# Optimization experiments

Measured on AMD Instinct MI355X. Metric: run time of the kernel, lower is better.

The kernel has to match this reference:

```python
import jax, jax.numpy as jnp
import numpy as np

S = 2048      # words in the sentence
LMAX = 16     # max chars per word (padded)
VOCAB = 50000
ALPHA = 256
CE = 256      # char_embedding_dim (also char-LSTM hidden)
WE = 512      # word_embedding_dim
H = 1024      # hidden_dim of word LSTM


def setup_inputs() -> dict:
    key = jax.random.key(0)
    ks = jax.random.split(key, 13)
    def u(k, shape, scale):
        return jax.random.uniform(k, shape, jnp.float32, -scale, scale)
    sc_c = 1.0 / np.sqrt(CE).astype(np.float32)   # torch LSTM init scale
    sc_w = 1.0 / np.sqrt(H).astype(np.float32)
    return {
        "word_idxs": jax.random.randint(ks[0], (S,), 0, VOCAB),
        "char_idxs": jax.random.randint(ks[1], (S, LMAX), 0, ALPHA),
        "char_lens": jax.random.randint(ks[2], (S,), 1, LMAX + 1),
        "char_emb": jax.random.normal(ks[3], (ALPHA, CE), jnp.float32) * 0.1,
        "word_emb": jax.random.normal(ks[4], (VOCAB, WE), jnp.float32) * 0.1,
        "Wih_c": u(ks[5], (4 * CE, CE), sc_c),
        "Whh_c": u(ks[6], (4 * CE, CE), sc_c),
        "bih_c": u(ks[7], (4 * CE,), sc_c),
        "bhh_c": u(ks[8], (4 * CE,), sc_c),
        "Wih_w": u(ks[9], (4 * H, WE + CE), sc_w),
        "Whh_w": u(ks[10], (4 * H, H), sc_w),
        "bih_w": u(ks[11], (4 * H,), sc_w),
        "bhh_w": u(ks[12], (4 * H,), sc_w),
    }


def _lstm_scan(xs, Wih, Whh, bih, bhh, hdim):
    """Single-layer LSTM, torch gate order (i, f, g, o). xs: [T, B, D] -> hs [T, B, hdim]."""
    B = xs.shape[1]
    bias = bih + bhh
    def step(carry, x):
        h, c = carry
        gates = x @ Wih.T + h @ Whh.T + bias  # [B, 4*hdim]
        i, f, g, o = jnp.split(gates, 4, axis=-1)
        c = jax.nn.sigmoid(f) * c + jax.nn.sigmoid(i) * jnp.tanh(g)
        h = jax.nn.sigmoid(o) * jnp.tanh(c)
        return (h, c), h
    init = (jnp.zeros((B, hdim), xs.dtype), jnp.zeros((B, hdim), xs.dtype))
    _, hs = jax.lax.scan(step, init, xs)
    return hs


def reference(word_idxs, char_idxs, char_lens, char_emb, word_emb,
              Wih_c, Whh_c, bih_c, bhh_c, Wih_w, Whh_w, bih_w, bhh_w):
    # Char LSTM: batch all S words together (fuses the per-word Python loop).
    # Causality makes output at t = len-1 identical to running the true-length seq.
    ce = char_emb[char_idxs]                  # [S, LMAX, CE]
    ce = jnp.swapaxes(ce, 0, 1)               # [LMAX, S, CE] time-major
    hs = _lstm_scan(ce, Wih_c, Whh_c, bih_c, bhh_c, CE)   # [LMAX, S, CE]
    hs = jnp.swapaxes(hs, 0, 1)               # [S, LMAX, CE]
    last = jnp.take_along_axis(hs, (char_lens - 1)[:, None, None], axis=1)[:, 0]  # [S, CE]

    we = word_emb[word_idxs]                  # [S, WE]
    lstm_in = jnp.concatenate([we, last], axis=-1)[:, None, :]  # [S, 1, WE+CE]
    out = _lstm_scan(lstm_in, Wih_w, Whh_w, bih_w, bhh_w, H)    # [S, 1, H]
    # dropout p=0.0 -> identity
    return out
```

## Files before the change

kernel.cpp:

```cpp
#include <hip/hip_runtime.h>
#include <stdint.h>

#define S_WORDS 2048
#define LMAX    16
#define CE      256
#define WE      512
#define HDIM    1024
#define GC      1024
#define GW      4096
#define KW      768
#define NWG_RNN 128
#define NWB_WIN 512
#define NMIR    4
#define RING_U64 (3 * HDIM)

#define IN_GATES_OFF 0
#define LAST_OFF     33554432
#define WT2C_OFF     35651584
#define WT2W_OFF     37748736
#define RING_OFF     WT2C_OFF
#define FLAGS_OFF    (RING_OFF + NMIR * RING_U64 * 8)

typedef float f32x4 __attribute__((ext_vector_type(4)));

#define LD_AGENT(p) __hip_atomic_load((p), __ATOMIC_RELAXED, __HIP_MEMORY_SCOPE_AGENT)

static __device__ __forceinline__ float sigm(float x) { return 1.0f / (1.0f + __expf(-x)); }
static __device__ __forceinline__ float tanh_fast(float x) {
    float ax = fminf(fabsf(x), 15.0f);
    float e  = __expf(2.0f * ax);
    float t  = (e - 1.0f) / (e + 1.0f);
    return copysignf(t, x);
}

__global__ void prep_c_kernel(const float* __restrict__ Wih,
                              const float* __restrict__ Whh,
                              float2* __restrict__ WT2c) {
    int idx = blockIdx.x * blockDim.x + threadIdx.x;
    if (idx >= 256 * GC) return;
    int kp = idx >> 10, row = idx & (GC - 1);
    int k = kp * 2;
    float2 v;
    if (k < CE) { v.x = Wih[row * CE + k];      v.y = Wih[row * CE + k + 1]; }
    else        { v.x = Whh[row * CE + k - CE]; v.y = Whh[row * CE + k - CE + 1]; }
    WT2c[idx] = v;
}

__global__ void prep_w_kernel(const float* __restrict__ Wih,
                              float2* __restrict__ WT2w) {
    int idx = blockIdx.x * blockDim.x + threadIdx.x;
    if (idx >= 384 * GW) return;
    int kp = idx >> 12, row = idx & (GW - 1);
    float2 v;
    v.x = Wih[row * KW + 2 * kp];
    v.y = Wih[row * KW + 2 * kp + 1];
    WT2w[idx] = v;
}

__global__ void __launch_bounds__(1024, 1) char_lstm_kernel(
    const int* __restrict__ char_idxs,
    const int* __restrict__ char_lens,
    const float* __restrict__ char_emb,
    const float* __restrict__ bih,
    const float* __restrict__ bhh,
    const float2* __restrict__ WT2c,
    float* __restrict__ last_out)
{
    __shared__ float xh[8][2 * CE];
    __shared__ float gex[4][256][9];
    const int j = threadIdx.x & 255;
    const int g = threadIdx.x >> 8;
    const int wbase = blockIdx.x * 8;

    const float bias = bih[g * CE + j] + bhh[g * CE + j];

    int len[2];
    float c[2] = {0.0f, 0.0f};
    len[0] = char_lens[wbase + 2 * g];
    len[1] = char_lens[wbase + 2 * g + 1];
    xh[2 * g][CE + j]     = 0.0f;
    xh[2 * g + 1][CE + j] = 0.0f;

    const float2* __restrict__ wrow = WT2c + g * CE + j;

    for (int t = 0; t < LMAX; t++) {
        {
            int ci0 = char_idxs[(wbase + 2 * g) * LMAX + t];
            int ci1 = char_idxs[(wbase + 2 * g + 1) * LMAX + t];
            xh[2 * g][j]     = char_emb[ci0 * CE + j];
            xh[2 * g + 1][j] = char_emb[ci1 * CE + j];
        }
        __syncthreads();

        float acc[8];
        #pragma unroll
        for (int w = 0; w < 8; w++) acc[w] = 0.0f;

        #pragma unroll 2
        for (int kq = 0; kq < 128; kq++) {
            float2 wv0 = wrow[(size_t)(2 * kq) * GC];
            float2 wv1 = wrow[(size_t)(2 * kq + 1) * GC];
            #pragma unroll
            for (int w = 0; w < 8; w++) {
                f32x4 xv = *(const f32x4*)&xh[w][4 * kq];
                acc[w] = fmaf(wv0.x, xv[0],
                         fmaf(wv0.y, xv[1],
                         fmaf(wv1.x, xv[2],
                         fmaf(wv1.y, xv[3], acc[w]))));
            }
        }

        #pragma unroll
        for (int w = 0; w < 8; w++) gex[g][j][w] = acc[w] + bias;
        __syncthreads();

        #pragma unroll
        for (int ww = 0; ww < 2; ww++) {
            int w = 2 * g + ww;
            float gi = gex[0][j][w];
            float gf = gex[1][j][w];
            float gg = gex[2][j][w];
            float go = gex[3][j][w];
            float iv = sigm(gi);
            float fv = sigm(gf);
            float gv = tanhf(gg);
            float ov = sigm(go);
            c[ww] = fv * c[ww] + iv * gv;
            float h = ov * tanhf(c[ww]);
            xh[w][CE + j] = h;
            if (t == len[ww] - 1) last_out[(wbase + w) * CE + j] = h;
        }
    }
}

__global__ void __launch_bounds__(512, 2) fused_word_kernel(
    const float* __restrict__ Whh,
    const int* __restrict__ word_idxs,
    const float* __restrict__ word_emb,
    const float* __restrict__ last,
    const float2* __restrict__ WT2w,
    const float* __restrict__ bih,
    const float* __restrict__ bhh,
    float* __restrict__ in_gates,
    unsigned long long* __restrict__ ring,
    unsigned int* __restrict__ flags,
    float* __restrict__ out)
{
    __shared__ float smem[8 * KW];
    const int tid = threadIdx.x;

    if (blockIdx.x >= NWG_RNN) {
        const int nb    = blockIdx.x - NWG_RNN;
        const int grp   = nb >> 1;
        const int half  = nb & 1;
        const int jj    = tid & 255;
        const int gh    = tid >> 8;
        const int rb2   = half * 2 + gh;
        const int wbase = grp * 8;
        float (*xh)[KW] = (float(*)[KW])smem;

        for (int w = 0; w < 8; w++) {
            int wi = word_idxs[wbase + w];
            xh[w][tid] = word_emb[(size_t)wi * WE + tid];
            if (tid < 256) xh[w][WE + tid] = last[(wbase + w) * CE + tid];
        }
        __syncthreads();

        float acc[4][8];
        #pragma unroll
        for (int g = 0; g < 4; g++)
            #pragma unroll
            for (int w = 0; w < 8; w++) acc[g][w] = 0.0f;

        for (int kp = 0; kp < KW / 2; kp++) {
            float2 wv[4];
            #pragma unroll
            for (int g = 0; g < 4; g++) wv[g] = WT2w[(size_t)kp * GW + rb2 * GC + g * CE + jj];
            #pragma unroll
            for (int w = 0; w < 8; w++) {
                float2 xv = *(const float2*)&xh[w][2 * kp];
                #pragma unroll
                for (int g = 0; g < 4; g++)
                    acc[g][w] = fmaf(wv[g].y, xv.y, fmaf(wv[g].x, xv.x, acc[g][w]));
            }
        }

        #pragma unroll
        for (int g = 0; g < 4; g++) {
            int row = rb2 * GC + g * CE + jj;
            float bias = bih[row] + bhh[row];
            #pragma unroll
            for (int w = 0; w < 8; w++)
                __hip_atomic_store(in_gates + (size_t)(wbase + w) * GW + row,
                                   acc[g][w] + bias,
                                   __ATOMIC_RELAXED, __HIP_MEMORY_SCOPE_AGENT);
        }
        __syncthreads();
        if (tid == 0)
            __hip_atomic_fetch_add(flags + grp, 1u,
                                   __ATOMIC_RELEASE, __HIP_MEMORY_SCOPE_AGENT);
        return;
    }

    const int v = tid >> 6;
    const int l = tid & 63;
    const int unit = blockIdx.x * 8 + v;
    float (*hbb)[HDIM] = (float(*)[HDIM])smem;
    const unsigned long long* ring_my = ring + (size_t)(blockIdx.x & (NMIR - 1)) * RING_U64;

    f32x4 w[4][4];
    #pragma unroll
    for (int g = 0; g < 4; g++)
        #pragma unroll
        for (int cc = 0; cc < 4; cc++)
            w[g][cc] = *(const f32x4*)(Whh + (size_t)(g * HDIM + unit) * HDIM
                                       + cc * 256 + l * 4);
    #pragma unroll
    for (int g = 0; g < 4; g++)
        #pragma unroll
        for (int cc = 0; cc < 4; cc++)
            asm volatile("" : "+v"(w[g][cc]));

    float c_reg = 0.0f;

    for (int t = 0; t < S_WORDS; t++) {
        if ((t & 7) == 0) {
            const unsigned int* fl = flags + (t >> 3);
            while (LD_AGENT(fl) < 2u) {}
        }

        float ing0 = 0.f, ing1 = 0.f, ing2 = 0.f, ing3 = 0.f;
        if (l < 4) {
            const float* ig = in_gates + (size_t)t * GW + unit;
            ing0 = LD_AGENT(ig + 0 * HDIM);
            ing1 = LD_AGENT(ig + 1 * HDIM);
            ing2 = LD_AGENT(ig + 2 * HDIM);
            ing3 = LD_AGENT(ig + 3 * HDIM);
        }

        const unsigned long long* slot = ring_my + (size_t)(t % 3) * HDIM + v * 128;
        unsigned long long a0 = 0, a1 = 0;
        bool ok0 = false, ok1 = false;
        do {
            if (!ok0) {
                a0 = LD_AGENT(slot + l);
                ok0 = ((unsigned)(a0 >> 32) == (unsigned)t);
            }
            if (!ok1) {
                a1 = LD_AGENT(slot + 64 + l);
                ok1 = ((unsigned)(a1 >> 32) == (unsigned)t);
            }
        } while (!__all(ok0 && ok1));
        {
            union { unsigned u32; float f; } c0, c1;
            c0.u32 = (unsigned)a0; c1.u32 = (unsigned)a1;
            hbb[t & 1][v * 128 + l]      = c0.f;
            hbb[t & 1][v * 128 + 64 + l] = c1.f;
        }
        __syncthreads();

        float acc0 = 0.f, acc1 = 0.f, acc2 = 0.f, acc3 = 0.f;
        const float* hb = hbb[t & 1];
        #pragma unroll
        for (int cc = 0; cc < 4; cc++) {
            f32x4 hv = *(const f32x4*)&hb[cc * 256 + l * 4];
            #pragma unroll
            for (int e = 0; e < 4; e++) {
                acc0 = fmaf(w[0][cc][e], hv[e], acc0);
                acc1 = fmaf(w[1][cc][e], hv[e], acc1);
                acc2 = fmaf(w[2][cc][e], hv[e], acc2);
                acc3 = fmaf(w[3][cc][e], hv[e], acc3);
            }
        }
        #pragma unroll
        for (int off = 32; off >= 1; off >>= 1) {
            acc0 += __shfl_xor(acc0, off, 64);
            acc1 += __shfl_xor(acc1, off, 64);
            acc2 += __shfl_xor(acc2, off, 64);
            acc3 += __shfl_xor(acc3, off, 64);
        }

        if (l < 4) {
            float iv = sigm(acc0 + ing0);
            float fv = sigm(acc1 + ing1);
            float gv = tanh_fast(acc2 + ing2);
            float ov = sigm(acc3 + ing3);
            c_reg = fv * c_reg + iv * gv;
            float h = ov * tanh_fast(c_reg);
            union { float f; unsigned u32; } cv; cv.f = h;
            unsigned long long pv =
                ((unsigned long long)(unsigned)(t + 1) << 32) | (unsigned long long)cv.u32;
            __hip_atomic_store(ring + (size_t)l * RING_U64
                                    + (size_t)((t + 1) % 3) * HDIM + unit, pv,
                               __ATOMIC_RELAXED, __HIP_MEMORY_SCOPE_AGENT);
            if (l == 0) out[(size_t)t * HDIM + unit] = h;
        }
    }
}

extern "C" void kernel_launch(void* const* d_in, const int* in_sizes, int n_in,
                              void* d_out, int out_size, void* d_ws, size_t ws_size,
                              hipStream_t stream) {
    const int* word_idxs = (const int*)d_in[0];
    const int* char_idxs = (const int*)d_in[1];
    const int* char_lens = (const int*)d_in[2];
    const float* char_emb = (const float*)d_in[3];
    const float* word_emb = (const float*)d_in[4];
    const float* Wih_c = (const float*)d_in[5];
    const float* Whh_c = (const float*)d_in[6];
    const float* bih_c = (const float*)d_in[7];
    const float* bhh_c = (const float*)d_in[8];
    const float* Wih_w = (const float*)d_in[9];
    const float* Whh_w = (const float*)d_in[10];
    const float* bih_w = (const float*)d_in[11];
    const float* bhh_w = (const float*)d_in[12];

    char* ws = (char*)d_ws;
    float*  in_gates = (float*)(ws + IN_GATES_OFF);
    float*  last     = (float*)(ws + LAST_OFF);
    float2* WT2c     = (float2*)(ws + WT2C_OFF);
    float2* WT2w     = (float2*)(ws + WT2W_OFF);
    unsigned long long* ring = (unsigned long long*)(ws + RING_OFF);
    unsigned int* flags      = (unsigned int*)(ws + FLAGS_OFF);

    hipLaunchKernelGGL(prep_c_kernel, dim3(1024), dim3(256), 0, stream,
                       Wih_c, Whh_c, WT2c);
    hipLaunchKernelGGL(prep_w_kernel, dim3(6144), dim3(256), 0, stream,
                       Wih_w, WT2w);
    hipLaunchKernelGGL(char_lstm_kernel, dim3(256), dim3(1024), 0, stream,
                       char_idxs, char_lens, char_emb, bih_c, bhh_c, WT2c, last);
    hipMemsetAsync(ws + RING_OFF, 0,
                   NMIR * RING_U64 * sizeof(unsigned long long) + 256 * sizeof(unsigned int),
                   stream);
    hipLaunchKernelGGL(fused_word_kernel, dim3(NWG_RNN + NWB_WIN), dim3(512), 0, stream,
                       Whh_w, word_idxs, word_emb, last, WT2w, bih_w, bhh_w,
                       in_gates, ring, flags, (float*)d_out);
}
```

Baseline: 5.514 ms.

## Drop Wih_w transpose kernel and read original layout; software-pipeline char LSTM weight loads

```diff
diff --git a/kernel.cpp b/kernel.cpp
--- a/kernel.cpp
+++ b/kernel.cpp
@@ -17,7 +17,6 @@
 #define IN_GATES_OFF 0
 #define LAST_OFF     33554432
 #define WT2C_OFF     35651584
-#define WT2W_OFF     37748736
 #define RING_OFF     WT2C_OFF
 #define FLAGS_OFF    (RING_OFF + NMIR * RING_U64 * 8)
 
@@ -44,17 +43,6 @@
     if (k < CE) { v.x = Wih[row * CE + k];      v.y = Wih[row * CE + k + 1]; }
     else        { v.x = Whh[row * CE + k - CE]; v.y = Whh[row * CE + k - CE + 1]; }
     WT2c[idx] = v;
-}
-
-__global__ void prep_w_kernel(const float* __restrict__ Wih,
-                              float2* __restrict__ WT2w) {
-    int idx = blockIdx.x * blockDim.x + threadIdx.x;
-    if (idx >= 384 * GW) return;
-    int kp = idx >> 12, row = idx & (GW - 1);
-    float2 v;
-    v.x = Wih[row * KW + 2 * kp];
-    v.y = Wih[row * KW + 2 * kp + 1];
-    WT2w[idx] = v;
 }
 
 __global__ void __launch_bounds__(1024, 1) char_lstm_kernel(
@@ -96,18 +84,30 @@
         #pragma unroll
         for (int w = 0; w < 8; w++) acc[w] = 0.0f;
 
-        #pragma unroll 2
-        for (int kq = 0; kq < 128; kq++) {
-            float2 wv0 = wrow[(size_t)(2 * kq) * GC];
-            float2 wv1 = wrow[(size_t)(2 * kq + 1) * GC];
+        float2 c0 = wrow[0 * GC], c1 = wrow[1 * GC];
+        float2 d0 = wrow[2 * GC], d1 = wrow[3 * GC];
+        const float2* wp = wrow + 4 * GC;
+        for (int kq = 0; kq < 128; kq += 2) {
+            float2 e0 = wp[0 * GC], e1 = wp[1 * GC];
+            float2 f0 = wp[2 * GC], f1 = wp[3 * GC];
+            wp += 4 * GC;
             #pragma unroll
             for (int w = 0; w < 8; w++) {
                 f32x4 xv = *(const f32x4*)&xh[w][4 * kq];
-                acc[w] = fmaf(wv0.x, xv[0],
-                         fmaf(wv0.y, xv[1],
-                         fmaf(wv1.x, xv[2],
-                         fmaf(wv1.y, xv[3], acc[w]))));
-            }
+                acc[w] = fmaf(c0.x, xv[0],
+                         fmaf(c0.y, xv[1],
+                         fmaf(c1.x, xv[2],
+                         fmaf(c1.y, xv[3], acc[w]))));
+            }
+            #pragma unroll
+            for (int w = 0; w < 8; w++) {
+                f32x4 xv = *(const f32x4*)&xh[w][4 * kq + 4];
+                acc[w] = fmaf(d0.x, xv[0],
+                         fmaf(d0.y, xv[1],
+                         fmaf(d1.x, xv[2],
+                         fmaf(d1.y, xv[3], acc[w]))));
+            }
+            c0 = e0; c1 = e1; d0 = f0; d1 = f1;
         }
 
         #pragma unroll
@@ -138,7 +138,7 @@
     const int* __restrict__ word_idxs,
     const float* __restrict__ word_emb,
     const float* __restrict__ last,
-    const float2* __restrict__ WT2w,
+    const float* __restrict__ Wih_w,
     const float* __restrict__ bih,
     const float* __restrict__ bhh,
     float* __restrict__ in_gates,
@@ -166,22 +166,33 @@
         }
         __syncthreads();
 
+        const float* wr0 = Wih_w + (size_t)(rb2 * GC + 0 * CE + jj) * KW;
+        const float* wr1 = Wih_w + (size_t)(rb2 * GC + 1 * CE + jj) * KW;
+        const float* wr2 = Wih_w + (size_t)(rb2 * GC + 2 * CE + jj) * KW;
+        const float* wr3 = Wih_w + (size_t)(rb2 * GC + 3 * CE + jj) * KW;
+
         float acc[4][8];
         #pragma unroll
         for (int g = 0; g < 4; g++)
             #pragma unroll
             for (int w = 0; w < 8; w++) acc[g][w] = 0.0f;
 
-        for (int kp = 0; kp < KW / 2; kp++) {
-            float2 wv[4];
-            #pragma unroll
-            for (int g = 0; g < 4; g++) wv[g] = WT2w[(size_t)kp * GW + rb2 * GC + g * CE + jj];
+        for (int kq = 0; kq < KW / 4; kq++) {
+            f32x4 w0 = *(const f32x4*)(wr0 + 4 * kq);
+            f32x4 w1 = *(const f32x4*)(wr1 + 4 * kq);
+            f32x4 w2 = *(const f32x4*)(wr2 + 4 * kq);
+            f32x4 w3 = *(const f32x4*)(wr3 + 4 * kq);
             #pragma unroll
             for (int w = 0; w < 8; w++) {
-                float2 xv = *(const float2*)&xh[w][2 * kp];
-                #pragma unroll
-                for (int g = 0; g < 4; g++)
-                    acc[g][w] = fmaf(wv[g].y, xv.y, fmaf(wv[g].x, xv.x, acc[g][w]));
+                f32x4 xv = *(const f32x4*)&xh[w][4 * kq];
+                acc[0][w] = fmaf(w0[0], xv[0], fmaf(w0[1], xv[1],
+                            fmaf(w0[2], xv[2], fmaf(w0[3], xv[3], acc[0][w]))));
+                acc[1][w] = fmaf(w1[0], xv[0], fmaf(w1[1], xv[1],
+                            fmaf(w1[2], xv[2], fmaf(w1[3], xv[3], acc[1][w]))));
+                acc[2][w] = fmaf(w2[0], xv[0], fmaf(w2[1], xv[1],
+                            fmaf(w2[2], xv[2], fmaf(w2[3], xv[3], acc[2][w]))));
+                acc[3][w] = fmaf(w3[0], xv[0], fmaf(w3[1], xv[1],
+                            fmaf(w3[2], xv[2], fmaf(w3[3], xv[3], acc[3][w]))));
             }
         }
 
@@ -319,20 +330,17 @@
     float*  in_gates = (float*)(ws + IN_GATES_OFF);
     float*  last     = (float*)(ws + LAST_OFF);
     float2* WT2c     = (float2*)(ws + WT2C_OFF);
-    float2* WT2w     = (float2*)(ws + WT2W_OFF);
     unsigned long long* ring = (unsigned long long*)(ws + RING_OFF);
     unsigned int* flags      = (unsigned int*)(ws + FLAGS_OFF);
 
     hipLaunchKernelGGL(prep_c_kernel, dim3(1024), dim3(256), 0, stream,
                        Wih_c, Whh_c, WT2c);
-    hipLaunchKernelGGL(prep_w_kernel, dim3(6144), dim3(256), 0, stream,
-                       Wih_w, WT2w);
     hipLaunchKernelGGL(char_lstm_kernel, dim3(256), dim3(1024), 0, stream,
                        char_idxs, char_lens, char_emb, bih_c, bhh_c, WT2c, last);
     hipMemsetAsync(ws + RING_OFF, 0,
                    NMIR * RING_U64 * sizeof(unsigned long long) + 256 * sizeof(unsigned int),
                    stream);
     hipLaunchKernelGGL(fused_word_kernel, dim3(NWG_RNN + NWB_WIN), dim3(512), 0, stream,
-                       Whh_w, word_idxs, word_emb, last, WT2w, bih_w, bhh_w,
+                       Whh_w, word_idxs, word_emb, last, Wih_w, bih_w, bhh_w,
                        in_gates, ring, flags, (float*)d_out);
 }
```

Result: slower. 6.023 ms (+9.2%).

## Replicate char-LSTM weights per XCD, early-exit on max length, prefetch weights

Applied to the files above, without the earlier changes.

```diff
diff --git a/kernel.cpp b/kernel.cpp
--- a/kernel.cpp
+++ b/kernel.cpp
@@ -15,10 +15,11 @@
 #define RING_U64 (3 * HDIM)
 
 #define IN_GATES_OFF 0
+#define WTREP_OFF    0
 #define LAST_OFF     33554432
-#define WT2C_OFF     35651584
+#define RINGREG_OFF  35651584
 #define WT2W_OFF     37748736
-#define RING_OFF     WT2C_OFF
+#define RING_OFF     RINGREG_OFF
 #define FLAGS_OFF    (RING_OFF + NMIR * RING_U64 * 8)
 
 typedef float f32x4 __attribute__((ext_vector_type(4)));
@@ -35,7 +36,7 @@
 
 __global__ void prep_c_kernel(const float* __restrict__ Wih,
                               const float* __restrict__ Whh,
-                              float2* __restrict__ WT2c) {
+                              float2* __restrict__ WTrep) {
     int idx = blockIdx.x * blockDim.x + threadIdx.x;
     if (idx >= 256 * GC) return;
     int kp = idx >> 10, row = idx & (GC - 1);
@@ -43,7 +44,9 @@
     float2 v;
     if (k < CE) { v.x = Wih[row * CE + k];      v.y = Wih[row * CE + k + 1]; }
     else        { v.x = Whh[row * CE + k - CE]; v.y = Whh[row * CE + k - CE + 1]; }
-    WT2c[idx] = v;
+    #pragma unroll
+    for (int c = 0; c < 8; c++)
+        WTrep[(size_t)c * (256 * GC) + idx] = v;
 }
 
 __global__ void prep_w_kernel(const float* __restrict__ Wih,
@@ -63,7 +66,7 @@
     const float* __restrict__ char_emb,
     const float* __restrict__ bih,
     const float* __restrict__ bhh,
-    const float2* __restrict__ WT2c,
+    const float2* __restrict__ WTrep,
     float* __restrict__ last_out)
 {
     __shared__ float xh[8][2 * CE];
@@ -78,12 +81,19 @@
     float c[2] = {0.0f, 0.0f};
     len[0] = char_lens[wbase + 2 * g];
     len[1] = char_lens[wbase + 2 * g + 1];
+    int tmax = 1;
+    #pragma unroll
+    for (int w = 0; w < 8; w++) {
+        int lw = char_lens[wbase + w];
+        tmax = lw > tmax ? lw : tmax;
+    }
     xh[2 * g][CE + j]     = 0.0f;
     xh[2 * g + 1][CE + j] = 0.0f;
 
-    const float2* __restrict__ wrow = WT2c + g * CE + j;
-
-    for (int t = 0; t < LMAX; t++) {
+    const float2* __restrict__ wrow =
+        WTrep + (size_t)(blockIdx.x & 7) * (256 * GC) + g * CE + j;
+
+    for (int t = 0; t < tmax; t++) {
         {
             int ci0 = char_idxs[(wbase + 2 * g) * LMAX + t];
             int ci1 = char_idxs[(wbase + 2 * g + 1) * LMAX + t];
@@ -96,18 +106,30 @@
         #pragma unroll
         for (int w = 0; w < 8; w++) acc[w] = 0.0f;
 
-        #pragma unroll 2
-        for (int kq = 0; kq < 128; kq++) {
-            float2 wv0 = wrow[(size_t)(2 * kq) * GC];
-            float2 wv1 = wrow[(size_t)(2 * kq + 1) * GC];
+        float2 c0 = wrow[0 * GC], c1 = wrow[1 * GC];
+        float2 d0 = wrow[2 * GC], d1 = wrow[3 * GC];
+        const float2* wp = wrow + 4 * GC;
+        for (int kq = 0; kq < 128; kq += 2) {
+            float2 e0 = wp[0 * GC], e1 = wp[1 * GC];
+            float2 f0 = wp[2 * GC], f1 = wp[3 * GC];
+            wp += 4 * GC;
             #pragma unroll
             for (int w = 0; w < 8; w++) {
                 f32x4 xv = *(const f32x4*)&xh[w][4 * kq];
-                acc[w] = fmaf(wv0.x, xv[0],
-                         fmaf(wv0.y, xv[1],
-                         fmaf(wv1.x, xv[2],
-                         fmaf(wv1.y, xv[3], acc[w]))));
-            }
+                acc[w] = fmaf(c0.x, xv[0],
+                         fmaf(c0.y, xv[1],
+                         fmaf(c1.x, xv[2],
+                         fmaf(c1.y, xv[3], acc[w]))));
+            }
+            #pragma unroll
+            for (int w = 0; w < 8; w++) {
+                f32x4 xv = *(const f32x4*)&xh[w][4 * kq + 4];
+                acc[w] = fmaf(d0.x, xv[0],
+                         fmaf(d0.y, xv[1],
+                         fmaf(d1.x, xv[2],
+                         fmaf(d1.y, xv[3], acc[w]))));
+            }
+            c0 = e0; c1 = e1; d0 = f0; d1 = f1;
         }
 
         #pragma unroll
@@ -317,18 +339,18 @@
 
     char* ws = (char*)d_ws;
     float*  in_gates = (float*)(ws + IN_GATES_OFF);
+    float2* WTrep    = (float2*)(ws + WTREP_OFF);
     float*  last     = (float*)(ws + LAST_OFF);
-    float2* WT2c     = (float2*)(ws + WT2C_OFF);
     float2* WT2w     = (float2*)(ws + WT2W_OFF);
     unsigned long long* ring = (unsigned long long*)(ws + RING_OFF);
     unsigned int* flags      = (unsigned int*)(ws + FLAGS_OFF);
 
     hipLaunchKernelGGL(prep_c_kernel, dim3(1024), dim3(256), 0, stream,
-                       Wih_c, Whh_c, WT2c);
+                       Wih_c, Whh_c, WTrep);
     hipLaunchKernelGGL(prep_w_kernel, dim3(6144), dim3(256), 0, stream,
                        Wih_w, WT2w);
     hipLaunchKernelGGL(char_lstm_kernel, dim3(256), dim3(1024), 0, stream,
-                       char_idxs, char_lens, char_emb, bih_c, bhh_c, WT2c, last);
+                       char_idxs, char_lens, char_emb, bih_c, bhh_c, WTrep, last);
     hipMemsetAsync(ws + RING_OFF, 0,
                    NMIR * RING_U64 * sizeof(unsigned long long) + 256 * sizeof(unsigned int),
                    stream);
```

Result: no change. 5.536 ms (+0.4%).
